# Performance work log

Hardware: AMD Instinct MI355X
Metric: run time of the kernel (lower is better)

Reference implementation:

```python
import jax, jax.numpy as jnp
import numpy as np

N = 524288
B, F, H, W = 2, 4, 64, 512
S = B * F * H * W  # dense voxel segment space
EPS = 1e-5


def _bn(x, g, b):
    # BatchNorm1d in training mode: normalize over the point dim with biased var
    m = x.mean(0)
    v = jnp.mean((x - m) ** 2, 0)
    return (x - m) / jnp.sqrt(v + EPS) * g + b


def setup_inputs() -> dict:
    key = jax.random.key(0)
    ks = jax.random.split(key, 20)
    pts = jax.random.normal(ks[0], (N, 4), dtype=jnp.float32) * 10.0
    bcol = jax.random.randint(ks[1], (N, 1), 0, B)
    fcol = jax.random.randint(ks[2], (N, 1), 0, F)
    hcol = jax.random.randint(ks[3], (N, 1), 0, H)
    wcol = jax.random.randint(ks[4], (N, 1), 0, W)
    coors = jnp.concatenate([bcol, fcol, hcol, wcol], -1).astype(jnp.int32)
    # original reads batch_size/frame_size from coors[-1]
    coors = coors.at[-1].set(jnp.array([B - 1, F - 1, H - 1, W - 1], dtype=jnp.int32))
    s = 0.02
    p = {
        'pre_gamma': jnp.ones((8,), jnp.float32),
        'pre_beta': jnp.zeros((8,), jnp.float32),
        'W1': jax.random.normal(ks[5], (8, 64), jnp.float32) * s,
        'g1': jnp.ones((64,), jnp.float32), 'b1': jnp.zeros((64,), jnp.float32),
        'W2': jax.random.normal(ks[6], (64, 128), jnp.float32) * s,
        'g2': jnp.ones((128,), jnp.float32), 'b2': jnp.zeros((128,), jnp.float32),
        'W3': jax.random.normal(ks[7], (128, 256), jnp.float32) * s,
        'g3': jnp.ones((256,), jnp.float32), 'b3': jnp.zeros((256,), jnp.float32),
        'W4': jax.random.normal(ks[8], (256, 256), jnp.float32) * s,
        'b4': jnp.zeros((256,), jnp.float32),
        'Wc': jax.random.normal(ks[9], (256, 64), jnp.float32) * s,
        'bc': jnp.zeros((64,), jnp.float32),
    }
    return {'pts': pts, 'pts_coors': coors, **p}


def reference(pts, pts_coors, pre_gamma, pre_beta, W1, g1, b1, W2, g2, b2,
              W3, g3, b3, W4, b4, Wc, bc):
    c = pts_coors
    lin = ((c[:, 0] * F + c[:, 1]) * H + c[:, 2]) * W + c[:, 3]  # (N,)
    counts = jax.ops.segment_sum(jnp.ones((pts.shape[0],), pts.dtype), lin, num_segments=S)
    # with_distance
    dist = jnp.linalg.norm(pts[:, :3], axis=1, keepdims=True)
    # with_cluster_center: scatter_mean then gather
    vsum = jax.ops.segment_sum(pts, lin, num_segments=S)
    vmean = vsum / jnp.clip(counts, 1.0)[:, None]
    f_cluster = pts[:, :3] - vmean[lin][:, :3]
    feats = jnp.concatenate([pts, dist, f_cluster], -1)  # (N, 8)
    feats = _bn(feats, pre_gamma, pre_beta)  # pre_norm
    x = jax.nn.relu(_bn(feats @ W1, g1, b1))
    x = jax.nn.relu(_bn(x @ W2, g2, b2))
    x = jax.nn.relu(_bn(x @ W3, g3, b3))
    point_feats = x @ W4 + b4  # (N, 256)
    # scatter_max over voxels
    seg = jax.ops.segment_max(point_feats, lin, num_segments=S)
    mask = (counts > 0)[:, None]
    voxel_feats = jnp.where(mask, seg, 0.0)
    comp = jax.nn.relu(voxel_feats @ Wc + bc)
    comp = jnp.where(mask, comp, 0.0)  # empty voxels stay zero in stack_frame
    stack = comp.reshape(B, F, H, W, -1)  # (B, F, H, W, Cc)
    residual = jnp.concatenate([stack[:, -1] - stack[:, f] for f in range(F - 1)], -1)
    residual_img = jnp.transpose(residual, (0, 3, 1, 2))  # (B, C, H, W)
    return residual_img
```

## Files before the change

kernel.cpp:

```cpp
#include <hip/hip_runtime.h>
#include <hip/hip_bf16.h>
#include <stdint.h>

typedef unsigned int u32;
typedef unsigned short u16;
typedef __attribute__((ext_vector_type(8))) short bf16x8;
typedef __attribute__((ext_vector_type(4))) float f32x4;

#define NPTS 524288
#define FF 4
#define HH 64
#define WW 512
#define SS 262144
#define EPSV 1e-5f
#define NB 8192
#define RCAP 80
#define VCAP 80

__device__ __forceinline__ float bf2f(u16 h){ return __uint_as_float(((u32)h)<<16); }
__device__ __forceinline__ u16 f2bf(float f){
  u32 u = __float_as_uint(f);
  return (u16)((u + 0x7FFFu + ((u>>16)&1u)) >> 16);
}

__device__ __forceinline__ void point_feats(int p, const float* __restrict__ pts,
    const u32* __restrict__ lin, const u32* __restrict__ counts,
    const float* __restrict__ vsum, float f[8], u32* vout){
  float4 pt = ((const float4*)pts)[p];
  u32 v = lin[p];
  float cnt = fmaxf((float)counts[v], 1.0f);
  float inv = 1.0f/cnt;
  float mx = vsum[v*3+0]*inv, my = vsum[v*3+1]*inv, mz = vsum[v*3+2]*inv;
  float dist = sqrtf(pt.x*pt.x + pt.y*pt.y + pt.z*pt.z);
  f[0]=pt.x; f[1]=pt.y; f[2]=pt.z; f[3]=pt.w; f[4]=dist;
  f[5]=pt.x-mx; f[6]=pt.y-my; f[7]=pt.z-mz;
  *vout = v;
}

__global__ __launch_bounds__(256) void k_lin(const float* __restrict__ pts,
                                             const int* __restrict__ coors,
                                             u32* __restrict__ lin,
                                             u32* __restrict__ counts,
                                             float* __restrict__ vsum){
  int p = blockIdx.x*256 + threadIdx.x;
  int4 c = ((const int4*)coors)[p];
  u32 v = ((u32)((c.x*FF + c.y)*HH + c.z))*WW + (u32)c.w;
  lin[p] = v;
  atomicAdd(&counts[v], 1u);
  float4 pt = ((const float4*)pts)[p];
  atomicAdd(&vsum[v*3+0], pt.x);
  atomicAdd(&vsum[v*3+1], pt.y);
  atomicAdd(&vsum[v*3+2], pt.z);
}

__global__ __launch_bounds__(256) void k_scan_a(const u32* __restrict__ counts,
                                                u32* __restrict__ blockSums){
  __shared__ u32 lds[256];
  int b = blockIdx.x, t = threadIdx.x;
  uint4 c4 = ((const uint4*)counts)[b*256 + t];
  lds[t] = c4.x + c4.y + c4.z + c4.w;
  __syncthreads();
  for(int s=128; s>0; s>>=1){ if(t<s) lds[t] += lds[t+s]; __syncthreads(); }
  if(t==0) blockSums[b] = lds[0];
}

__global__ void k_scan_b(u32* blockSums){
  if(threadIdx.x==0){
    u32 run = 0;
    for(int i=0;i<256;i++){ u32 v = blockSums[i]; blockSums[i] = run; run += v; }
  }
}

__global__ __launch_bounds__(256) void k_scan_c(const u32* __restrict__ counts,
                                                const u32* __restrict__ blockSums,
                                                u32* __restrict__ offsets,
                                                u32* __restrict__ cursor){
  __shared__ u32 lds[256];
  int b = blockIdx.x, t = threadIdx.x;
  uint4 c4 = ((const uint4*)counts)[b*256 + t];
  u32 mysum = c4.x + c4.y + c4.z + c4.w;
  lds[t] = mysum;
  __syncthreads();
  for(int d=1; d<256; d<<=1){
    u32 v = (t>=d) ? lds[t-d] : 0u;
    __syncthreads();
    lds[t] += v;
    __syncthreads();
  }
  u32 off = blockSums[b] + (t>0 ? lds[t-1] : 0u);
  u32 base = (u32)(b*1024 + t*4);
  offsets[base+0]=off; cursor[base+0]=off; off += c4.x;
  offsets[base+1]=off; cursor[base+1]=off; off += c4.y;
  offsets[base+2]=off; cursor[base+2]=off; off += c4.z;
  offsets[base+3]=off; cursor[base+3]=off; off += c4.w;
  if(base+4 == SS) offsets[SS] = off;
}

__global__ __launch_bounds__(256) void k_scatter(const u32* __restrict__ lin,
                                                 u32* __restrict__ cursor,
                                                 u32* __restrict__ order){
  int p = blockIdx.x*256 + threadIdx.x;
  u32 v = lin[p];
  u32 pos = atomicAdd(&cursor[v], 1u);
  order[pos] = p;
}

__global__ __launch_bounds__(256) void k_prep(const float* __restrict__ W2,
    const float* __restrict__ W3, const float* __restrict__ W4,
    const float* __restrict__ Wc,
    u16* __restrict__ W2t, u16* __restrict__ W3t, u16* __restrict__ W4t,
    u16* __restrict__ Wct){
  int i = blockIdx.x*256 + threadIdx.x;
  if(i < 8192){
    int k = i >> 7, n = i & 127;
    W2t[n*64 + k] = f2bf(W2[i]);
  } else if(i < 8192+32768){
    int j = i - 8192;
    int k = j >> 8, n = j & 255;
    W3t[n*128 + k] = f2bf(W3[j]);
  } else if(i < 8192+32768+65536){
    int j = i - (8192+32768);
    int k = j >> 8, n = j & 255;
    W4t[n*256 + k] = f2bf(W4[j]);
  } else if(i < 8192+32768+65536+16384){
    int j = i - (8192+32768+65536);
    int k = j >> 6, n = j & 63;
    Wct[n*256 + k] = f2bf(Wc[j]);
  }
}

__global__ __launch_bounds__(256) void k_stats0(const float* __restrict__ pts,
    const u32* __restrict__ lin, const u32* __restrict__ counts,
    const float* __restrict__ vsum, float* __restrict__ sum0, float* __restrict__ sq0){
  int p = blockIdx.x*256 + threadIdx.x;
  float f[8]; u32 v;
  point_feats(p, pts, lin, counts, vsum, f, &v);
  __shared__ float lsum[4][8], lsq[4][8];
  int lane = threadIdx.x & 63, wv = threadIdx.x >> 6;
  #pragma unroll
  for(int c=0;c<8;c++){
    float s = f[c], q = f[c]*f[c];
    #pragma unroll
    for(int d=32; d; d>>=1){ s += __shfl_xor(s,d); q += __shfl_xor(q,d); }
    if(lane==0){ lsum[wv][c]=s; lsq[wv][c]=q; }
  }
  __syncthreads();
  if(threadIdx.x<8){
    float s=0.f,q=0.f;
    for(int g=0;g<4;g++){ s+=lsum[g][threadIdx.x]; q+=lsq[g][threadIdx.x]; }
    atomicAdd(&sum0[threadIdx.x], s);
    atomicAdd(&sq0[threadIdx.x], q);
  }
}

__global__ void k_fold(const float* __restrict__ sum, const float* __restrict__ sq,
                       const float* __restrict__ g, const float* __restrict__ b,
                       float* __restrict__ a, float* __restrict__ c, int C){
  int i = blockIdx.x*64 + threadIdx.x;
  if(i < C){
    float m = sum[i]*(1.0f/NPTS);
    float v = sq[i]*(1.0f/NPTS) - m*m;
    v = fmaxf(v, 0.0f);
    float ai = g[i] / sqrtf(v + EPSV);
    a[i] = ai;
    c[i] = b[i] - m*ai;
  }
}

__global__ __launch_bounds__(256) void k_stats1(const float* __restrict__ pts,
    const u32* __restrict__ lin, const u32* __restrict__ counts,
    const float* __restrict__ vsum,
    const float* __restrict__ a0, const float* __restrict__ c0,
    const float* __restrict__ W1, float* __restrict__ sum1, float* __restrict__ sq1){
  __shared__ float ws[4][64], wq[4][64];
  int t = threadIdx.x;
  int p = blockIdx.x*256 + t;
  float f[8]; u32 v;
  point_feats(p, pts, lin, counts, vsum, f, &v);
  float y0[8];
  #pragma unroll
  for(int k=0;k<8;k++) y0[k] = a0[k]*f[k] + c0[k];
  float z[64];
  #pragma unroll
  for(int j=0;j<64;j++){
    float s=0.f;
    #pragma unroll
    for(int k=0;k<8;k++) s += y0[k]*W1[k*64+j];
    z[j]=s;
  }
  int lane = t&63, wv = t>>6;
  float ks=0.f, kq=0.f;
  #pragma unroll
  for(int c=0;c<64;c++){
    float s=z[c], q=z[c]*z[c];
    #pragma unroll
    for(int d=1; d<64; d<<=1){ s+=__shfl_xor(s,d); q+=__shfl_xor(q,d); }
    if(lane==c){ ks=s; kq=q; }
  }
  ws[wv][lane]=ks; wq[wv][lane]=kq;
  __syncthreads();
  if(t<64){
    float S=ws[0][t]+ws[1][t]+ws[2][t]+ws[3][t];
    float Q=wq[0][t]+wq[1][t]+wq[2][t]+wq[3][t];
    atomicAdd(&sum1[t],S); atomicAdd(&sq1[t],Q);
  }
}

__global__ __launch_bounds__(256,2) void k_mstats2(
    const float* __restrict__ pts, const u32* __restrict__ lin,
    const u32* __restrict__ counts, const float* __restrict__ vsum,
    const float* __restrict__ a0, const float* __restrict__ c0,
    const float* __restrict__ a1, const float* __restrict__ c1,
    const float* __restrict__ W1, const u16* __restrict__ W2t,
    float* __restrict__ sum2, float* __restrict__ sq2){
  __shared__ u16 T1[256*72];
  int tid = threadIdx.x, lane = tid&63, wid = tid>>6, l15 = lane&15, lg = lane>>4;
  float s2[2] = {0.f,0.f}, q2[2] = {0.f,0.f};

  for(int cch=0; cch<4; cch++){
    int p = blockIdx.x*1024 + cch*256 + tid;
    float f[8]; u32 v;
    point_feats(p, pts, lin, counts, vsum, f, &v);
    float y0[8];
    #pragma unroll
    for(int k=0;k<8;k++) y0[k] = a0[k]*f[k] + c0[k];
    u32 pk[32];
    #pragma unroll
    for(int jj=0;jj<32;jj++){
      float s0=0.f, s1=0.f;
      #pragma unroll
      for(int k=0;k<8;k++){ s0 += y0[k]*W1[k*64+2*jj]; s1 += y0[k]*W1[k*64+2*jj+1]; }
      float v0f = fmaxf(a1[2*jj]*s0   + c1[2*jj],   0.f);
      float v1f = fmaxf(a1[2*jj+1]*s1 + c1[2*jj+1], 0.f);
      pk[jj] = (u32)f2bf(v0f) | ((u32)f2bf(v1f)<<16);
    }
    __syncthreads();
    {
      uint4* dst = (uint4*)&T1[tid*72];
      #pragma unroll
      for(int q=0;q<8;q++) dst[q] = make_uint4(pk[4*q],pk[4*q+1],pk[4*q+2],pk[4*q+3]);
    }
    __syncthreads();
    #pragma unroll
    for(int ci=0; ci<2; ci++){
      int ch = (wid + 4*ci)*16 + l15;
      const u16* wb = W2t + (size_t)ch*64 + lg*8;
      bf16x8 b0 = *(const bf16x8*)(wb);
      bf16x8 b1 = *(const bf16x8*)(wb + 32);
      for(int rt=0; rt<16; rt++){
        const u16* ap = T1 + (rt*16 + l15)*72 + lg*8;
        bf16x8 af0 = *(const bf16x8*)(ap);
        bf16x8 af1 = *(const bf16x8*)(ap + 32);
        f32x4 acc = {0.f,0.f,0.f,0.f};
        acc = __builtin_amdgcn_mfma_f32_16x16x32_bf16(af0, b0, acc, 0,0,0);
        acc = __builtin_amdgcn_mfma_f32_16x16x32_bf16(af1, b1, acc, 0,0,0);
        #pragma unroll
        for(int i=0;i<4;i++){ s2[ci] += acc[i]; q2[ci] += acc[i]*acc[i]; }
      }
    }
  }
  #pragma unroll
  for(int ci=0; ci<2; ci++){
    float s = s2[ci], q = q2[ci];
    s += __shfl_xor(s,16); s += __shfl_xor(s,32);
    q += __shfl_xor(q,16); q += __shfl_xor(q,32);
    if(lg == 0){
      int ch = (wid + 4*ci)*16 + l15;
      atomicAdd(&sum2[ch], s);
      atomicAdd(&sq2[ch], q);
    }
  }
}

__global__ __launch_bounds__(256,1) void k_chain2(
    const float* __restrict__ pts, const u32* __restrict__ lin,
    const u32* __restrict__ counts, const float* __restrict__ vsum,
    const u32* __restrict__ order,
    const float* __restrict__ a0, const float* __restrict__ c0,
    const float* __restrict__ a1, const float* __restrict__ c1,
    const float* __restrict__ a2, const float* __restrict__ c2,
    const float* __restrict__ W1, const u16* __restrict__ W2t,
    const u16* __restrict__ W3t,
    u32* __restrict__ y2s,
    float* __restrict__ sum3, float* __restrict__ sq3){
  __shared__ u16 T1[256*72];
  __shared__ u16 T2[256*136];
  int tid = threadIdx.x, lane = tid&63, wid = tid>>6, l15 = lane&15, lg = lane>>4;
  float s3[4] = {0.f,0.f,0.f,0.f}, q3[4] = {0.f,0.f,0.f,0.f};

  for(int cch=0; cch<4; cch++){
    int rr = blockIdx.x*1024 + cch*256 + tid;
    int p = (int)order[rr];
    float f[8]; u32 v;
    point_feats(p, pts, lin, counts, vsum, f, &v);
    float y0[8];
    #pragma unroll
    for(int k=0;k<8;k++) y0[k] = a0[k]*f[k] + c0[k];
    u32 pk[32];
    #pragma unroll
    for(int jj=0;jj<32;jj++){
      float s0=0.f, s1=0.f;
      #pragma unroll
      for(int k=0;k<8;k++){ s0 += y0[k]*W1[k*64+2*jj]; s1 += y0[k]*W1[k*64+2*jj+1]; }
      float v0f = fmaxf(a1[2*jj]*s0   + c1[2*jj],   0.f);
      float v1f = fmaxf(a1[2*jj+1]*s1 + c1[2*jj+1], 0.f);
      pk[jj] = (u32)f2bf(v0f) | ((u32)f2bf(v1f)<<16);
    }
    __syncthreads();
    {
      uint4* dst = (uint4*)&T1[tid*72];
      #pragma unroll
      for(int q=0;q<8;q++) dst[q] = make_uint4(pk[4*q],pk[4*q+1],pk[4*q+2],pk[4*q+3]);
    }
    __syncthreads();
    #pragma unroll
    for(int ci=0; ci<2; ci++){
      int ch = (wid + 4*ci)*16 + l15;
      const u16* wb = W2t + (size_t)ch*64 + lg*8;
      bf16x8 b0 = *(const bf16x8*)(wb);
      bf16x8 b1 = *(const bf16x8*)(wb + 32);
      float a2v = a2[ch], c2v = c2[ch];
      for(int rt=0; rt<16; rt++){
        const u16* ap = T1 + (rt*16 + l15)*72 + lg*8;
        bf16x8 af0 = *(const bf16x8*)(ap);
        bf16x8 af1 = *(const bf16x8*)(ap + 32);
        f32x4 acc = {0.f,0.f,0.f,0.f};
        acc = __builtin_amdgcn_mfma_f32_16x16x32_bf16(af0, b0, acc, 0,0,0);
        acc = __builtin_amdgcn_mfma_f32_16x16x32_bf16(af1, b1, acc, 0,0,0);
        int rbase = rt*16 + lg*4;
        #pragma unroll
        for(int i=0;i<4;i++)
          T2[(rbase+i)*136 + ch] = f2bf(fmaxf(a2v*acc[i] + c2v, 0.f));
      }
    }
    __syncthreads();
    {
      const u32* T2w = (const u32*)T2;
      u32 base = (u32)blockIdx.x*1024u + (u32)cch*256u;
      for(int i=tid; i<256*64; i+=256){
        int row = i>>6, w = i&63;
        y2s[(size_t)(base+row)*64 + w] = T2w[row*68 + w];
      }
    }
    #pragma unroll
    for(int ci=0; ci<4; ci++){
      int ch = (wid + 4*ci)*16 + l15;
      const u16* wb = W3t + (size_t)ch*128 + lg*8;
      bf16x8 b[4];
      #pragma unroll
      for(int ks=0; ks<4; ks++) b[ks] = *(const bf16x8*)(wb + ks*32);
      for(int rt=0; rt<16; rt++){
        const u16* ap = T2 + (rt*16 + l15)*136 + lg*8;
        f32x4 acc = {0.f,0.f,0.f,0.f};
        #pragma unroll
        for(int ks=0; ks<4; ks++){
          bf16x8 af = *(const bf16x8*)(ap + ks*32);
          acc = __builtin_amdgcn_mfma_f32_16x16x32_bf16(af, b[ks], acc, 0,0,0);
        }
        #pragma unroll
        for(int i=0;i<4;i++){ s3[ci] += acc[i]; q3[ci] += acc[i]*acc[i]; }
      }
    }
  }
  #pragma unroll
  for(int ci=0; ci<4; ci++){
    float s = s3[ci], q = q3[ci];
    s += __shfl_xor(s,16); s += __shfl_xor(s,32);
    q += __shfl_xor(q,16); q += __shfl_xor(q,32);
    if(lg == 0){
      int ch = (wid + 4*ci)*16 + l15;
      atomicAdd(&sum3[ch], s);
      atomicAdd(&sq3[ch], q);
    }
  }
}

__global__ __launch_bounds__(512,4) void k_z4(
    const u32* __restrict__ y2s,
    const float* __restrict__ a3, const float* __restrict__ c3,
    const u16* __restrict__ W3t, const u16* __restrict__ W4t,
    u16* __restrict__ z4t){
  __shared__ u16 T3[128*264];
  int tid = threadIdx.x, lane = tid & 63, wid = tid >> 6;
  int l15 = lane & 15, lg = lane >> 4;
  size_t row0 = (size_t)blockIdx.x * 128;

  for(int ci=0; ci<2; ci++){
    int ch = (wid + 8*ci)*16 + l15;
    const u16* wb = W3t + (size_t)ch*128 + lg*8;
    bf16x8 b[4];
    #pragma unroll
    for(int ks=0; ks<4; ks++) b[ks] = *(const bf16x8*)(wb + ks*32);
    float a3v = a3[ch], c3v = c3[ch];
    for(int rt=0; rt<8; rt++){
      const u16* ap = (const u16*)y2s + (row0 + rt*16 + l15)*128 + lg*8;
      f32x4 acc = {0.f,0.f,0.f,0.f};
      #pragma unroll
      for(int ks=0; ks<4; ks++){
        bf16x8 af = *(const bf16x8*)(ap + ks*32);
        acc = __builtin_amdgcn_mfma_f32_16x16x32_bf16(af, b[ks], acc, 0,0,0);
      }
      int rbase = rt*16 + lg*4;
      #pragma unroll
      for(int i=0;i<4;i++)
        T3[(rbase+i)*264 + ch] = f2bf(fmaxf(a3v*acc[i] + c3v, 0.f));
    }
  }
  __syncthreads();

  for(int ci=0; ci<2; ci++){
    int ch = (wid + 8*ci)*16 + l15;
    const u16* wb = W4t + (size_t)ch*256 + lg*8;
    bf16x8 b[8];
    #pragma unroll
    for(int ks=0; ks<8; ks++) b[ks] = *(const bf16x8*)(wb + ks*32);
    for(int rt=0; rt<8; rt++){
      const u16* ap = T3 + (rt*16 + l15)*264 + lg*8;
      f32x4 acc = {0.f,0.f,0.f,0.f};
      #pragma unroll
      for(int ks=0; ks<8; ks++){
        bf16x8 af = *(const bf16x8*)(ap + ks*32);
        acc = __builtin_amdgcn_mfma_f32_16x16x32_bf16(af, b[ks], acc, 0,0,0);
      }
      size_t r = row0 + (size_t)rt*16 + lg*4;
      u32 p0 = (u32)f2bf(acc[0]) | ((u32)f2bf(acc[1])<<16);
      u32 p1 = (u32)f2bf(acc[2]) | ((u32)f2bf(acc[3])<<16);
      u32* dst = (u32*)(z4t + (size_t)ch*NPTS + r);
      dst[0] = p0; dst[1] = p1;
    }
  }
}

__global__ __launch_bounds__(256,4) void k_segcomp(
    const u32* __restrict__ offsets, const u16* __restrict__ z4t,
    const float* __restrict__ b4, const u16* __restrict__ Wct,
    const float* __restrict__ bc, u16* __restrict__ comp){
  __shared__ u16 TA[64*264];
  __shared__ u32 voff[65];
  __shared__ float bb[256];
  int tid = threadIdx.x, lane = tid & 63, wid = tid >> 6;
  int l15 = lane & 15, lg = lane >> 4;
  u32 v0 = (u32)blockIdx.x * 64u;

  if(tid < 65) voff[tid] = offsets[v0 + tid];
  bb[tid] = b4[tid];
  __syncthreads();

  {
    int k = tid;
    const u16* col = z4t + (size_t)k*NPTS;
    for(int v=0; v<64; v++){
      u32 r0 = voff[v], r1 = voff[v+1];
      u16 o = 0;
      if(r1 > r0){
        float m = -3.0e38f;
        for(u32 r=r0; r<r1; r++) m = fmaxf(m, bf2f(col[r]));
        o = f2bf(m + bb[k]);
      }
      TA[v*264 + k] = o;
    }
  }
  __syncthreads();

  int ch4 = wid*16 + l15;
  const u16* wb = Wct + (size_t)ch4*256 + lg*8;
  bf16x8 b[8];
  #pragma unroll
  for(int ks=0; ks<8; ks++) b[ks] = *(const bf16x8*)(wb + ks*32);
  float bcv = bc[ch4];
  #pragma unroll
  for(int vt=0; vt<4; vt++){
    const u16* ap = TA + (vt*16 + l15)*264 + lg*8;
    f32x4 acc = {0.f,0.f,0.f,0.f};
    #pragma unroll
    for(int ks=0; ks<8; ks++){
      bf16x8 af = *(const bf16x8*)(ap + ks*32);
      acc = __builtin_amdgcn_mfma_f32_16x16x32_bf16(af, b[ks], acc, 0,0,0);
    }
    int vbase = vt*16 + lg*4;
    #pragma unroll
    for(int i=0;i<4;i++){
      int vox = vbase + i;
      bool nz = voff[vox+1] > voff[vox];
      float val = nz ? fmaxf(acc[i] + bcv, 0.f) : 0.f;
      comp[(size_t)(v0+vox)*64 + ch4] = f2bf(val);
    }
  }
}

__global__ __launch_bounds__(256,2) void k_mega4(
    const u32* __restrict__ offsets, const u32* __restrict__ y2s,
    const float* __restrict__ a3, const float* __restrict__ c3,
    const u16* __restrict__ W3t, const u16* __restrict__ W4t,
    const u16* __restrict__ Wct,
    const float* __restrict__ b4, const float* __restrict__ bc,
    u16* __restrict__ comp){
  __shared__ __align__(16) char SM[65664];
  u16* T3  = (u16*)(SM);
  u16* T2s = (u16*)(SM + 42240);
  u16* Tz  = (u16*)(SM + 42240);
  u16* TA  = (u16*)(SM + 53760);
  u32* vst = (u32*)(SM + 65280);
  u32* hdr = (u32*)(SM + 65616);

  int tid = threadIdx.x, lane = tid & 63, wid = tid >> 6;
  int l15 = lane & 15, lg = lane >> 4;

  if(tid == 0){
    u32 t0 = (u32)blockIdx.x * 64u;
    u32 lo=0, hi=SS;
    while(lo<hi){ u32 mid=(lo+hi)>>1; if(offsets[mid] < t0) lo=mid+1; else hi=mid; }
    u32 vlo = lo, vhi;
    if(blockIdx.x == NB-1) vhi = SS;
    else {
      u32 t1 = t0 + 64u;
      lo = vlo; hi = SS;
      while(lo<hi){ u32 mid=(lo+hi)>>1; if(offsets[mid] < t1) lo=mid+1; else hi=mid; }
      vhi = lo;
    }
    hdr[0]=vlo; hdr[1]=vhi; hdr[2]=offsets[vlo]; hdr[3]=offsets[vhi];
  }
  __syncthreads();
  u32 vlo=hdr[0], vhi=hdr[1], start=hdr[2], end=hdr[3];
  int R = (int)(end - start); if(R > RCAP) R = RCAP;
  int V = (int)(vhi - vlo);   if(V > VCAP) V = VCAP;

  if(tid <= VCAP){
    u32 o = (tid <= V) ? offsets[vlo + tid] : end;
    int s = (int)(o - start); if(s > RCAP) s = RCAP;
    vst[tid] = (u32)s;
  }

  {
    u32* T2w = (u32*)T2s;
    for(int i=tid; i<RCAP*64; i+=256){
      int row = i>>6, w = i&63;
      u32 val = (row < R) ? y2s[(size_t)(start+row)*64 + w] : 0u;
      T2w[row*68 + w] = val;
    }
  }
  __syncthreads();

  for(int ci=0; ci<4; ci++){
    int ch = (wid + 4*ci)*16 + l15;
    const u16* wb = W3t + (size_t)ch*128 + lg*8;
    bf16x8 b[4];
    #pragma unroll
    for(int ks=0; ks<4; ks++) b[ks] = *(const bf16x8*)(wb + ks*32);
    float a3v = a3[ch], c3v = c3[ch];
    for(int rt=0; rt<5; rt++){
      const u16* ap = T2s + (rt*16 + l15)*136 + lg*8;
      f32x4 acc = {0.f,0.f,0.f,0.f};
      #pragma unroll
      for(int ks=0; ks<4; ks++){
        bf16x8 af = *(const bf16x8*)(ap + ks*32);
        acc = __builtin_amdgcn_mfma_f32_16x16x32_bf16(af, b[ks], acc, 0,0,0);
      }
      int rbase = rt*16 + lg*4;
      #pragma unroll
      for(int i=0;i<4;i++)
        T3[(rbase+i)*264 + ch] = f2bf(fmaxf(a3v*acc[i] + c3v, 0.f));
    }
  }
  __syncthreads();

  f32x4 acc5[5];
  #pragma unroll
  for(int i=0;i<5;i++) acc5[i] = (f32x4){0.f,0.f,0.f,0.f};
  int ch4 = wid*16 + l15;

  for(int oc=0; oc<4; oc++){
    {
      int chg = oc*64 + ch4;
      const u16* wb = W4t + (size_t)chg*256 + lg*8;
      bf16x8 b[8];
      #pragma unroll
      for(int ks=0; ks<8; ks++) b[ks] = *(const bf16x8*)(wb + ks*32);
      for(int rt=0; rt<5; rt++){
        const u16* ap = T3 + (rt*16 + l15)*264 + lg*8;
        f32x4 acc = {0.f,0.f,0.f,0.f};
        #pragma unroll
        for(int ks=0; ks<8; ks++){
          bf16x8 af = *(const bf16x8*)(ap + ks*32);
          acc = __builtin_amdgcn_mfma_f32_16x16x32_bf16(af, b[ks], acc, 0,0,0);
        }
        int rbase = rt*16 + lg*4;
        #pragma unroll
        for(int i=0;i<4;i++)
          Tz[(rbase+i)*72 + ch4] = f2bf(acc[i]);
      }
    }
    __syncthreads();
    for(int i=tid; i<VCAP*64; i+=256){
      int v = i>>6, k = i&63;
      u32 r0 = vst[v], r1 = vst[v+1];
      u16 outv = 0;
      if(r1 > r0){
        float m = -3.0e38f;
        for(u32 r=r0; r<r1; r++) m = fmaxf(m, bf2f(Tz[r*72+k]));
        outv = f2bf(m + b4[oc*64+k]);
      }
      TA[v*72+k] = outv;
    }
    __syncthreads();
    {
      const u16* wb = Wct + (size_t)ch4*256 + oc*64 + lg*8;
      bf16x8 b0 = *(const bf16x8*)(wb);
      bf16x8 b1 = *(const bf16x8*)(wb + 32);
      #pragma unroll
      for(int vt=0; vt<5; vt++){
        const u16* ap = TA + (vt*16 + l15)*72 + lg*8;
        bf16x8 af0 = *(const bf16x8*)(ap);
        bf16x8 af1 = *(const bf16x8*)(ap + 32);
        acc5[vt] = __builtin_amdgcn_mfma_f32_16x16x32_bf16(af0, b0, acc5[vt], 0,0,0);
        acc5[vt] = __builtin_amdgcn_mfma_f32_16x16x32_bf16(af1, b1, acc5[vt], 0,0,0);
      }
    }
    __syncthreads();
  }

  {
    float bcv = bc[ch4];
    #pragma unroll
    for(int vt=0; vt<5; vt++){
      int vbase = vt*16 + lg*4;
      #pragma unroll
      for(int i=0;i<4;i++){
        int vox = vbase + i;
        if(vox < V){
          bool nz = vst[vox+1] > vst[vox];
          float val = nz ? fmaxf(acc5[vt][i] + bcv, 0.f) : 0.f;
          comp[(size_t)(vlo+vox)*64 + ch4] = f2bf(val);
        }
      }
    }
  }
}

__global__ __launch_bounds__(256) void k_resid(const u16* __restrict__ comp,
                                               float* __restrict__ out){
  __shared__ u32 cl[4*128*32];
  int t = threadIdx.x;
  int blk = blockIdx.x;
  int wq = blk & 3, h = (blk>>2) & 63, b = blk>>8;
  int w0 = wq*128;
  for(int fr=0; fr<4; fr++){
    const u32* src = (const u32*)comp + ((size_t)(((b*4+fr)*64 + h)*512 + w0))*32;
    for(int i=t; i<4096; i+=256){
      int vox = i>>5, wd = i&31;
      cl[fr*4096 + vox*32 + (wd ^ (vox&31))] = src[i];
    }
  }
  __syncthreads();
  int wl = t & 127, half = t >> 7;
  int mv = wl & 31;
  for(int ch = half; ch < 64; ch += 2){
    u32 wr3 = cl[3*4096 + wl*32 + ((ch>>1) ^ mv)];
    float r3 = bf2f((ch&1) ? (u16)(wr3>>16) : (u16)(wr3&0xFFFFu));
    #pragma unroll
    for(int fr=0; fr<3; fr++){
      u32 wrf = cl[fr*4096 + wl*32 + ((ch>>1) ^ mv)];
      float vf = bf2f((ch&1) ? (u16)(wrf>>16) : (u16)(wrf&0xFFFFu));
      out[(((size_t)(b*192 + fr*64 + ch))*64 + h)*512 + w0 + wl] = r3 - vf;
    }
  }
}

extern "C" void kernel_launch(void* const* d_in, const int* in_sizes, int n_in,
                              void* d_out, int out_size, void* d_ws, size_t ws_size,
                              hipStream_t stream){
  const float* pts  = (const float*)d_in[0];
  const int*  coors = (const int*)d_in[1];
  const float* g0 = (const float*)d_in[2];
  const float* b0 = (const float*)d_in[3];
  const float* W1 = (const float*)d_in[4];
  const float* g1 = (const float*)d_in[5];
  const float* b1 = (const float*)d_in[6];
  const float* W2 = (const float*)d_in[7];
  const float* g2 = (const float*)d_in[8];
  const float* b2 = (const float*)d_in[9];
  const float* W3 = (const float*)d_in[10];
  const float* g3 = (const float*)d_in[11];
  const float* b3 = (const float*)d_in[12];
  const float* W4 = (const float*)d_in[13];
  const float* b4 = (const float*)d_in[14];
  const float* Wc = (const float*)d_in[15];
  const float* bc = (const float*)d_in[16];
  float* out = (float*)d_out;
  (void)in_sizes; (void)n_in; (void)out_size;

  char* ws = (char*)d_ws;
  size_t off = 0;
  auto alloc = [&](size_t bytes)->void*{
    void* p = ws + off;
    off += (bytes + 255) & ~(size_t)255;
    return p;
  };
  u32*  counts  = (u32*)alloc((size_t)SS*4);
  float* vsum   = (float*)alloc((size_t)SS*3*4);
  float* stats  = (float*)alloc(8192);
  size_t zero_bytes = off;
  u32*  lin     = (u32*)alloc((size_t)NPTS*4);
  u32*  offsets = (u32*)alloc((size_t)(SS+1)*4);
  u32*  cursor  = (u32*)alloc((size_t)SS*4);
  u32*  order   = (u32*)alloc((size_t)NPTS*4);
  u32*  blockSums = (u32*)alloc(1024);
  u16*  comp    = (u16*)alloc((size_t)SS*64*2);
  u16*  W2t = (u16*)alloc(8192*2);
  u16*  W3t = (u16*)alloc(32768*2);
  u16*  W4t = (u16*)alloc(65536*2);
  u16*  Wct = (u16*)alloc(16384*2);
  u32*  y2s = (u32*)alloc((size_t)NPTS*64*4);
  u16*  z4t = (u16*)alloc((size_t)NPTS*256*2);
  bool use_split = (off <= ws_size);

  float* sum0=stats+0,   *sq0=stats+8,    *a0=stats+16,   *c0=stats+24;
  float* sum1=stats+32,  *sq1=stats+96,   *a1=stats+160,  *c1=stats+224;
  float* sum2=stats+288, *sq2=stats+416,  *a2=stats+544,  *c2=stats+672;
  float* sum3=stats+800, *sq3=stats+1056, *a3=stats+1312, *c3=stats+1568;

  hipMemsetAsync(d_ws, 0, zero_bytes, stream);

  k_prep   <<<480, 256,0,stream>>>(W2, W3, W4, Wc, W2t, W3t, W4t, Wct);
  k_lin    <<<2048,256,0,stream>>>(pts, coors, lin, counts, vsum);
  k_scan_a <<<256, 256,0,stream>>>(counts, blockSums);
  k_scan_b <<<1,   64, 0,stream>>>(blockSums);
  k_scan_c <<<256, 256,0,stream>>>(counts, blockSums, offsets, cursor);
  k_scatter<<<2048,256,0,stream>>>(lin, cursor, order);

  k_stats0 <<<2048,256,0,stream>>>(pts, lin, counts, vsum, sum0, sq0);
  k_fold   <<<1,   64, 0,stream>>>(sum0, sq0, g0, b0, a0, c0, 8);
  k_stats1 <<<2048,256,0,stream>>>(pts, lin, counts, vsum, a0, c0, W1, sum1, sq1);
  k_fold   <<<1,   64, 0,stream>>>(sum1, sq1, g1, b1, a1, c1, 64);
  k_mstats2<<<512, 256,0,stream>>>(pts, lin, counts, vsum, a0,c0,a1,c1, W1, W2t, sum2, sq2);
  k_fold   <<<2,   64, 0,stream>>>(sum2, sq2, g2, b2, a2, c2, 128);
  k_chain2 <<<512, 256,0,stream>>>(pts, lin, counts, vsum, order,
                                   a0,c0,a1,c1,a2,c2, W1, W2t, W3t,
                                   y2s, sum3, sq3);
  k_fold   <<<4,   64, 0,stream>>>(sum3, sq3, g3, b3, a3, c3, 256);

  if(use_split){
    k_z4     <<<4096,512,0,stream>>>(y2s, a3, c3, W3t, W4t, z4t);
    k_segcomp<<<4096,256,0,stream>>>(offsets, z4t, b4, Wct, bc, comp);
  } else {
    k_mega4  <<<NB,  256,0,stream>>>(offsets, y2s, a3,c3, W3t, W4t, Wct, b4, bc, comp);
  }
  k_resid  <<<512, 256,0,stream>>>(comp, out);
}
```

Before: 1.191 ms.

## Chunk z4 GEMM and segment-max into voxel-range passes with small row-major buffer

Replaces the full-size transposed z4 intermediate with a loop over 8 or 16 voxel ranges. Each pass computes z4 only for the rows in that range into a compact row-major buffer, then runs segment max and the compaction GEMM on it. The aim is to keep the intermediate small enough to stay cache-resident and avoid a full HBM round-trip of the N×256 tensor. The cost is many more kernel launches, bounds checks, and a tail of idle blocks, because each pass is launched with a grid sized for its row cap. A __syncthreads in the mega4 fallback loop is also removed, which may introduce a race on that path.

```diff
diff --git a/kernel.cpp b/kernel.cpp
--- a/kernel.cpp
+++ b/kernel.cpp
@@ -375,15 +375,19 @@
   }
 }
 
-__global__ __launch_bounds__(512,4) void k_z4(
-    const u32* __restrict__ y2s,
+__global__ __launch_bounds__(512,2) void k_z4b(
+    const u32* __restrict__ y2s, const u32* __restrict__ offsets,
+    u32 vbase, u32 vend, u32 caprows,
     const float* __restrict__ a3, const float* __restrict__ c3,
     const u16* __restrict__ W3t, const u16* __restrict__ W4t,
-    u16* __restrict__ z4t){
+    u16* __restrict__ z4){
   __shared__ u16 T3[128*264];
   int tid = threadIdx.x, lane = tid & 63, wid = tid >> 6;
   int l15 = lane & 15, lg = lane >> 4;
-  size_t row0 = (size_t)blockIdx.x * 128;
+  u32 rlo = offsets[vbase], rhi = offsets[vend];
+  u32 rows = rhi - rlo; if(rows > caprows) rows = caprows;
+  u32 row0 = (u32)blockIdx.x * 128u;
+  if(row0 >= rows) return;
 
   for(int ci=0; ci<2; ci++){
     int ch = (wid + 8*ci)*16 + l15;
@@ -393,7 +397,7 @@
     for(int ks=0; ks<4; ks++) b[ks] = *(const bf16x8*)(wb + ks*32);
     float a3v = a3[ch], c3v = c3[ch];
     for(int rt=0; rt<8; rt++){
-      const u16* ap = (const u16*)y2s + (row0 + rt*16 + l15)*128 + lg*8;
+      const u16* ap = (const u16*)y2s + ((size_t)rlo + row0 + rt*16 + l15)*128 + lg*8;
       f32x4 acc = {0.f,0.f,0.f,0.f};
       #pragma unroll
       for(int ks=0; ks<4; ks++){
@@ -422,17 +426,18 @@
         bf16x8 af = *(const bf16x8*)(ap + ks*32);
         acc = __builtin_amdgcn_mfma_f32_16x16x32_bf16(af, b[ks], acc, 0,0,0);
       }
-      size_t r = row0 + (size_t)rt*16 + lg*4;
-      u32 p0 = (u32)f2bf(acc[0]) | ((u32)f2bf(acc[1])<<16);
-      u32 p1 = (u32)f2bf(acc[2]) | ((u32)f2bf(acc[3])<<16);
-      u32* dst = (u32*)(z4t + (size_t)ch*NPTS + r);
-      dst[0] = p0; dst[1] = p1;
-    }
-  }
-}
-
-__global__ __launch_bounds__(256,4) void k_segcomp(
-    const u32* __restrict__ offsets, const u16* __restrict__ z4t,
+      u32 rb = row0 + (u32)(rt*16 + lg*4);
+      #pragma unroll
+      for(int i=0;i<4;i++){
+        u32 r = rb + (u32)i;
+        if(r < rows) z4[(size_t)r*256 + ch] = f2bf(acc[i]);
+      }
+    }
+  }
+}
+
+__global__ __launch_bounds__(256,4) void k_segcompb(
+    const u32* __restrict__ offsets, const u16* __restrict__ z4, u32 vbase,
     const float* __restrict__ b4, const u16* __restrict__ Wct,
     const float* __restrict__ bc, u16* __restrict__ comp){
   __shared__ u16 TA[64*264];
@@ -440,21 +445,21 @@
   __shared__ float bb[256];
   int tid = threadIdx.x, lane = tid & 63, wid = tid >> 6;
   int l15 = lane & 15, lg = lane >> 4;
-  u32 v0 = (u32)blockIdx.x * 64u;
+  u32 v0 = vbase + (u32)blockIdx.x * 64u;
 
   if(tid < 65) voff[tid] = offsets[v0 + tid];
   bb[tid] = b4[tid];
+  u32 rlo = offsets[vbase];
   __syncthreads();
 
   {
     int k = tid;
-    const u16* col = z4t + (size_t)k*NPTS;
     for(int v=0; v<64; v++){
       u32 r0 = voff[v], r1 = voff[v+1];
       u16 o = 0;
       if(r1 > r0){
         float m = -3.0e38f;
-        for(u32 r=r0; r<r1; r++) m = fmaxf(m, bf2f(col[r]));
+        for(u32 r=r0; r<r1; r++) m = fmaxf(m, bf2f(z4[(size_t)(r - rlo)*256 + k]));
         o = f2bf(m + bb[k]);
       }
       TA[v*264 + k] = o;
@@ -477,10 +482,10 @@
       bf16x8 af = *(const bf16x8*)(ap + ks*32);
       acc = __builtin_amdgcn_mfma_f32_16x16x32_bf16(af, b[ks], acc, 0,0,0);
     }
-    int vbase = vt*16 + lg*4;
+    int vbaseL = vt*16 + lg*4;
     #pragma unroll
     for(int i=0;i<4;i++){
-      int vox = vbase + i;
+      int vox = vbaseL + i;
       bool nz = voff[vox+1] > voff[vox];
       float val = nz ? fmaxf(acc[i] + bcv, 0.f) : 0.f;
       comp[(size_t)(v0+vox)*64 + ch4] = f2bf(val);
@@ -616,7 +621,6 @@
         acc5[vt] = __builtin_amdgcn_mfma_f32_16x16x32_bf16(af1, b1, acc5[vt], 0,0,0);
       }
     }
-    __syncthreads();
   }
 
   {
@@ -711,8 +715,14 @@
   u16*  W4t = (u16*)alloc(65536*2);
   u16*  Wct = (u16*)alloc(16384*2);
   u32*  y2s = (u32*)alloc((size_t)NPTS*64*4);
-  u16*  z4t = (u16*)alloc((size_t)NPTS*256*2);
-  bool use_split = (off <= ws_size);
+
+  int NE = 0; u32 caprows = 0; u16* z4buf = (u16*)(ws + off);
+  {
+    size_t cap8  = (size_t)(NPTS/8  + 8192);
+    size_t cap16 = (size_t)(NPTS/16 + 8192);
+    if(off + cap8*512  <= ws_size){ NE = 8;  caprows = (u32)cap8; }
+    else if(off + cap16*512 <= ws_size){ NE = 16; caprows = (u32)cap16; }
+  }
 
   float* sum0=stats+0,   *sq0=stats+8,    *a0=stats+16,   *c0=stats+24;
   float* sum1=stats+32,  *sq1=stats+96,   *a1=stats+160,  *c1=stats+224;
@@ -739,9 +749,16 @@
                                    y2s, sum3, sq3);
   k_fold   <<<4,   64, 0,stream>>>(sum3, sq3, g3, b3, a3, c3, 256);
 
-  if(use_split){
-    k_z4     <<<4096,512,0,stream>>>(y2s, a3, c3, W3t, W4t, z4t);
-    k_segcomp<<<4096,256,0,stream>>>(offsets, z4t, b4, Wct, bc, comp);
+  if(NE > 0){
+    u32 vstep = (u32)(SS / NE);
+    int gz = (int)((caprows + 127) / 128);
+    int gv = (int)(vstep / 64);
+    for(int e=0; e<NE; e++){
+      u32 vb = (u32)e * vstep, ve = vb + vstep;
+      k_z4b     <<<gz, 512,0,stream>>>(y2s, offsets, vb, ve, caprows,
+                                       a3, c3, W3t, W4t, z4buf);
+      k_segcompb<<<gv, 256,0,stream>>>(offsets, z4buf, vb, b4, Wct, bc, comp);
+    }
   } else {
     k_mega4  <<<NB,  256,0,stream>>>(offsets, y2s, a3,c3, W3t, W4t, Wct, b4, bc, comp);
   }
```

Result: slower. 1.895 ms (+59.1%).
